# Kernel optimization log

Measured on AMD Instinct MI355X. Metric: run time of the kernel, lower is better.

The kernel has to match this reference:

```python
import jax, jax.numpy as jnp
import numpy as np

MARGIN = 0.2
EPS = 1e-8


def setup_inputs() -> dict:
    key = jax.random.key(0)
    k1, k2, k3 = jax.random.split(key, 3)
    B, D, T, C = 4096, 512, 65536, 100
    batch = jax.random.normal(k1, (B, D), dtype=jnp.float32)
    beta = jnp.ones((C,), dtype=jnp.float32) * 1.2  # learned per-class beta param
    labels = jax.random.randint(k2, (B,), 0, C)
    triplets = jax.random.randint(k3, (T, 3), 0, B)
    return {"batch": batch, "beta": beta, "labels": labels, "triplets": triplets}


def reference(batch, beta, labels, triplets):
    # Gather anchor / positive / negative embeddings: [T, D]
    a = batch[triplets[:, 0]]
    p = batch[triplets[:, 1]]
    n = batch[triplets[:, 2]]
    d_ap = jnp.sqrt(jnp.sum((a - p) ** 2, axis=-1) + EPS)  # [T]
    d_an = jnp.sqrt(jnp.sum((a - n) ** 2, axis=-1) + EPS)  # [T]
    b = beta[labels[triplets[:, 0]]]  # per-anchor-class beta, [T]
    pos_loss = jax.nn.relu(d_ap - b + MARGIN)
    neg_loss = jax.nn.relu(b - d_an + MARGIN)
    # torch bool+bool is logical OR; count triplets with any active hinge
    pair_count = jnp.sum(((pos_loss > 0.0) | (neg_loss > 0.0)).astype(jnp.float32))
    total = jnp.sum(pos_loss + neg_loss)
    loss = jnp.where(pair_count > 0.0, total / jnp.maximum(pair_count, 1.0), total)
    return loss
```

## Files before the change

kernel.cpp:

```cpp
#include <hip/hip_runtime.h>

#define MARGIN 0.2f
#define EPS_    1e-8f
#define BM 128
#define BK 64

typedef __attribute__((ext_vector_type(8))) short short8;
typedef __attribute__((ext_vector_type(4))) float f32x4;

__device__ __forceinline__ unsigned pack_bf16(float lo, float hi)
{
    union { float f; unsigned u; } a, b;
    a.f = lo; b.f = hi;
    unsigned ua = (a.u + 0x7fffu + ((a.u >> 16) & 1u)) >> 16;
    unsigned ub = (b.u + 0x7fffu + ((b.u >> 16) & 1u)) & 0xffff0000u;
    return ua | ub;
}

__global__ __launch_bounds__(256) void prep_kernel(
    const float* __restrict__ in, uint4* __restrict__ out, int n8,
    float* __restrict__ ws_total, unsigned int* __restrict__ ws_cnt)
{
    int i = blockIdx.x * blockDim.x + threadIdx.x;
    if (i == 0) { *ws_total = 0.0f; *ws_cnt = 0u; }
    if (i < n8) {
        const float4 a = ((const float4*)in)[2 * i + 0];
        const float4 b = ((const float4*)in)[2 * i + 1];
        uint4 r;
        r.x = pack_bf16(a.x, a.y);
        r.y = pack_bf16(a.z, a.w);
        r.z = pack_bf16(b.x, b.y);
        r.w = pack_bf16(b.z, b.w);
        out[i] = r;
    }
}

__global__ __launch_bounds__(256) void gemm_xxt(
    const char* __restrict__ xb,
    float* __restrict__ G, int B, int D, int NB)
{
    int lin = blockIdx.x, bm = 0, rowlen = NB;
    while (lin >= rowlen) { lin -= rowlen; ++bm; --rowlen; }
    const int bn = bm + lin;

    __shared__ char At[2][BM * BK * 2];
    __shared__ char Bt[2][BM * BK * 2];
    const int tid  = threadIdx.x;
    const int lane = tid & 63;
    const int w    = tid >> 6;
    const int wr   = w >> 1, wc = w & 1;
    const int rowb = D * 2;

    f32x4 acc[4][4] = {};

    auto stage = [&](int kk, int p) {
        #pragma unroll
        for (int c4 = 0; c4 < 4; ++c4) {
            const int c = w * 4 + c4;
            const size_t arow = (size_t)bm * BM + c * 8 + (lane >> 3);
            const size_t brow = (size_t)bn * BM + c * 8 + (lane >> 3);
            const char* asrc = xb + arow * rowb + kk * (BK * 2) + (lane & 7) * 16;
            const char* bsrc = xb + brow * rowb + kk * (BK * 2) + (lane & 7) * 16;
            __builtin_amdgcn_global_load_lds((const unsigned*)asrc,
                (unsigned*)(At[p] + c * 1024 + lane * 16), 16, 0, 0);
            __builtin_amdgcn_global_load_lds((const unsigned*)bsrc,
                (unsigned*)(Bt[p] + c * 1024 + lane * 16), 16, 0, 0);
        }
    };

    const int nk = D / BK;
    stage(0, 0);
    for (int kk = 0; kk < nk; ++kk) {
        const int p = kk & 1;
        if (kk + 1 < nk) {
            stage(kk + 1, p ^ 1);
            asm volatile("s_waitcnt vmcnt(8)" ::: "memory");
        } else {
            asm volatile("s_waitcnt vmcnt(0)" ::: "memory");
        }
        __builtin_amdgcn_s_barrier();
        __builtin_amdgcn_sched_barrier(0);

        #pragma unroll
        for (int ks = 0; ks < 2; ++ks) {
            const int kbyte = ks * 64 + (lane >> 4) * 16;
            short8 a[4], b[4];
            #pragma unroll
            for (int m = 0; m < 4; ++m) {
                const int row = wr * 64 + m * 16 + (lane & 15);
                a[m] = *(const short8*)(At[p] + row * 128 + kbyte);
            }
            #pragma unroll
            for (int n = 0; n < 4; ++n) {
                const int row = wc * 64 + n * 16 + (lane & 15);
                b[n] = *(const short8*)(Bt[p] + row * 128 + kbyte);
            }
            #pragma unroll
            for (int m = 0; m < 4; ++m)
                #pragma unroll
                for (int n = 0; n < 4; ++n)
                    acc[m][n] = __builtin_amdgcn_mfma_f32_16x16x32_bf16(
                        a[m], b[n], acc[m][n], 0, 0, 0);
        }
        asm volatile("s_waitcnt lgkmcnt(0)" ::: "memory");
        __builtin_amdgcn_sched_barrier(0);
        __builtin_amdgcn_s_barrier();
    }

    #pragma unroll
    for (int m = 0; m < 4; ++m)
        #pragma unroll
        for (int n = 0; n < 4; ++n)
            #pragma unroll
            for (int j = 0; j < 4; ++j) {
                const int row = bm * BM + wr * 64 + m * 16 + (lane >> 4) * 4 + j;
                const int col = bn * BM + wc * 64 + n * 16 + (lane & 15);
                G[(size_t)row * B + col] = acc[m][n][j];
            }
}

__global__ __launch_bounds__(256) void tri_eval(
    const float* __restrict__ G,
    const float* __restrict__ beta,
    const int*   __restrict__ labels,
    const int*   __restrict__ trip,
    int B, int T,
    float*        __restrict__ ws_total,
    unsigned int* __restrict__ ws_cnt)
{
    const int i = blockIdx.x * blockDim.x + threadIdx.x;
    float pn = 0.0f;
    int   c  = 0;
    if (i < T) {
        const int t0 = trip[3 * i + 0];
        const int t1 = trip[3 * i + 1];
        const int t2 = trip[3 * i + 2];
        const int r1 = t0 < t1 ? t0 : t1, c1 = t0 < t1 ? t1 : t0;
        const int r2 = t0 < t2 ? t0 : t2, c2 = t0 < t2 ? t2 : t0;
        const float g01 = G[(size_t)r1 * B + c1];
        const float g02 = G[(size_t)r2 * B + c2];
        const float n0  = G[(size_t)t0 * B + t0];
        const float n1  = G[(size_t)t1 * B + t1];
        const float n2  = G[(size_t)t2 * B + t2];
        const float b   = beta[labels[t0]];
        const float dap = sqrtf(fmaxf(n0 + n1 - 2.0f * g01, 0.0f) + EPS_);
        const float dan = sqrtf(fmaxf(n0 + n2 - 2.0f * g02, 0.0f) + EPS_);
        const float pos = fmaxf(dap - b + MARGIN, 0.0f);
        const float neg = fmaxf(b - dan + MARGIN, 0.0f);
        pn = pos + neg;
        c  = ((pos > 0.0f) || (neg > 0.0f)) ? 1 : 0;
    }
    #pragma unroll
    for (int off = 1; off < 64; off <<= 1) {
        pn += __shfl_xor(pn, off, 64);
        c  += __shfl_xor(c,  off, 64);
    }
    __shared__ float s_tot[4];
    __shared__ int   s_cnt[4];
    const int wid = threadIdx.x >> 6;
    if ((threadIdx.x & 63) == 0) { s_tot[wid] = pn; s_cnt[wid] = c; }
    __syncthreads();
    if (threadIdx.x == 0) {
        atomicAdd(ws_total, s_tot[0] + s_tot[1] + s_tot[2] + s_tot[3]);
        atomicAdd(ws_cnt, (unsigned)(s_cnt[0] + s_cnt[1] + s_cnt[2] + s_cnt[3]));
    }
}

__global__ __launch_bounds__(256) void triplet_loss_generic(
    const float* __restrict__ batch,
    const float* __restrict__ beta,
    const int*   __restrict__ labels,
    const int*   __restrict__ triplets,
    int T, int D,
    float*        __restrict__ ws_total,
    unsigned int* __restrict__ ws_cnt)
{
    const int lane   = threadIdx.x & 63;
    const int wid    = threadIdx.x >> 6;
    const int gwave  = (blockIdx.x * blockDim.x + threadIdx.x) >> 6;
    const int nwaves = (gridDim.x * blockDim.x) >> 6;
    const int dq     = D >> 2;

    float        tot = 0.0f;
    unsigned int cnt = 0u;

    for (int t = gwave; t < T; t += nwaves) {
        const int t0 = triplets[3 * t + 0];
        const int t1 = triplets[3 * t + 1];
        const int t2 = triplets[3 * t + 2];
        const float4* A = (const float4*)(batch + (size_t)t0 * D);
        const float4* P = (const float4*)(batch + (size_t)t1 * D);
        const float4* N = (const float4*)(batch + (size_t)t2 * D);
        float sap = 0.0f, san = 0.0f;
        for (int idx = lane; idx < dq; idx += 64) {
            const float4 av = A[idx];
            const float4 pv = P[idx];
            const float4 nv = N[idx];
            float dx = av.x - pv.x, dy = av.y - pv.y, dz = av.z - pv.z, dw = av.w - pv.w;
            sap += dx * dx + dy * dy + dz * dz + dw * dw;
            dx = av.x - nv.x; dy = av.y - nv.y; dz = av.z - nv.z; dw = av.w - nv.w;
            san += dx * dx + dy * dy + dz * dz + dw * dw;
        }
        #pragma unroll
        for (int off = 1; off < 64; off <<= 1) {
            sap += __shfl_xor(sap, off, 64);
            san += __shfl_xor(san, off, 64);
        }
        if (lane == 0) {
            const float d_ap = sqrtf(sap + EPS_);
            const float d_an = sqrtf(san + EPS_);
            const float b    = beta[labels[t0]];
            const float pos  = fmaxf(d_ap - b + MARGIN, 0.0f);
            const float neg  = fmaxf(b - d_an + MARGIN, 0.0f);
            tot += pos + neg;
            cnt += ((pos > 0.0f) || (neg > 0.0f)) ? 1u : 0u;
        }
    }

    __shared__ float        s_tot[4];
    __shared__ unsigned int s_cnt[4];
    if (lane == 0) { s_tot[wid] = tot; s_cnt[wid] = cnt; }
    __syncthreads();
    if (threadIdx.x == 0) {
        float        bt = 0.0f;
        unsigned int bc = 0u;
        const int nw = blockDim.x >> 6;
        for (int i = 0; i < nw; ++i) { bt += s_tot[i]; bc += s_cnt[i]; }
        atomicAdd(ws_total, bt);
        atomicAdd(ws_cnt, bc);
    }
}

__global__ void finalize_kernel(const float* __restrict__ ws_total,
                                const unsigned int* __restrict__ ws_cnt,
                                float* __restrict__ out)
{
    const float total = ws_total[0];
    const float pc    = (float)ws_cnt[0];
    out[0] = (pc > 0.0f) ? (total / fmaxf(pc, 1.0f)) : total;
}

extern "C" void kernel_launch(void* const* d_in, const int* in_sizes, int n_in,
                              void* d_out, int out_size, void* d_ws, size_t ws_size,
                              hipStream_t stream)
{
    const float* batch    = (const float*)d_in[0];
    const float* beta     = (const float*)d_in[1];
    const int*   labels   = (const int*)d_in[2];
    const int*   triplets = (const int*)d_in[3];

    const int B = in_sizes[2];
    const int D = in_sizes[0] / B;
    const int T = in_sizes[3] / 3;

    float*        ws_total = (float*)d_ws;
    unsigned int* ws_cnt   = (unsigned int*)((char*)d_ws + sizeof(float));

    const size_t hb_off = 32768;
    const size_t g_off  = (hb_off + (size_t)B * D * 2 + 255) & ~(size_t)255;
    const size_t need   = g_off + (size_t)B * B * 4;

    const bool fast = (B % BM == 0) && (D % BK == 0) && (ws_size >= need) && (T >= 1);

    if (fast) {
        uint4* hb = (uint4*)((char*)d_ws + hb_off);
        float* G  = (float*)((char*)d_ws + g_off);

        const int n8 = (B * D) / 8;
        prep_kernel<<<(n8 + 255) / 256, 256, 0, stream>>>(
            batch, hb, n8, ws_total, ws_cnt);

        const int NB = B / BM;
        const int nblk = NB * (NB + 1) / 2;
        gemm_xxt<<<nblk, 256, 0, stream>>>((const char*)hb, G, B, D, NB);

        tri_eval<<<(T + 255) / 256, 256, 0, stream>>>(
            G, beta, labels, triplets, B, T, ws_total, ws_cnt);
    } else {
        (void)hipMemsetAsync(d_ws, 0, 2 * sizeof(float), stream);
        const int block = 256;
        int grid = 2048;
        const int max_grid = (T + 3) / 4;
        if (grid > max_grid) grid = max_grid;
        triplet_loss_generic<<<grid, block, 0, stream>>>(
            batch, beta, labels, triplets, T, D, ws_total, ws_cnt);
    }

    finalize_kernel<<<1, 1, 0, stream>>>(ws_total, ws_cnt, (float*)d_out);
}
```

Before: 49.91 us.

## Drop GEMM double buffering and fuse finalize into triplet eval via last-block counter

The GEMM now uses a single LDS buffer and waits for each tile's loads before computing, which halves shared memory use but removes load/compute overlap. The separate finalize kernel is removed in the fast path. The last tri_eval block, detected with an atomic done counter, writes the final loss instead. This saves a kernel launch at the cost of possible exposed memory latency in the GEMM.

```diff
diff --git a/kernel.cpp b/kernel.cpp
--- a/kernel.cpp
+++ b/kernel.cpp
@@ -19,10 +19,11 @@
 
 __global__ __launch_bounds__(256) void prep_kernel(
     const float* __restrict__ in, uint4* __restrict__ out, int n8,
-    float* __restrict__ ws_total, unsigned int* __restrict__ ws_cnt)
+    float* __restrict__ ws_total, unsigned int* __restrict__ ws_cnt,
+    unsigned int* __restrict__ ws_done)
 {
     int i = blockIdx.x * blockDim.x + threadIdx.x;
-    if (i == 0) { *ws_total = 0.0f; *ws_cnt = 0u; }
+    if (i == 0) { *ws_total = 0.0f; *ws_cnt = 0u; *ws_done = 0u; }
     if (i < n8) {
         const float4 a = ((const float4*)in)[2 * i + 0];
         const float4 b = ((const float4*)in)[2 * i + 1];
@@ -43,8 +44,8 @@
     while (lin >= rowlen) { lin -= rowlen; ++bm; --rowlen; }
     const int bn = bm + lin;
 
-    __shared__ char At[2][BM * BK * 2];
-    __shared__ char Bt[2][BM * BK * 2];
+    __shared__ char At[BM * BK * 2];
+    __shared__ char Bt[BM * BK * 2];
     const int tid  = threadIdx.x;
     const int lane = tid & 63;
     const int w    = tid >> 6;
@@ -53,7 +54,8 @@
 
     f32x4 acc[4][4] = {};
 
-    auto stage = [&](int kk, int p) {
+    const int nk = D / BK;
+    for (int kk = 0; kk < nk; ++kk) {
         #pragma unroll
         for (int c4 = 0; c4 < 4; ++c4) {
             const int c = w * 4 + c4;
@@ -62,22 +64,11 @@
             const char* asrc = xb + arow * rowb + kk * (BK * 2) + (lane & 7) * 16;
             const char* bsrc = xb + brow * rowb + kk * (BK * 2) + (lane & 7) * 16;
             __builtin_amdgcn_global_load_lds((const unsigned*)asrc,
-                (unsigned*)(At[p] + c * 1024 + lane * 16), 16, 0, 0);
+                (unsigned*)(At + c * 1024 + lane * 16), 16, 0, 0);
             __builtin_amdgcn_global_load_lds((const unsigned*)bsrc,
-                (unsigned*)(Bt[p] + c * 1024 + lane * 16), 16, 0, 0);
-        }
-    };
-
-    const int nk = D / BK;
-    stage(0, 0);
-    for (int kk = 0; kk < nk; ++kk) {
-        const int p = kk & 1;
-        if (kk + 1 < nk) {
-            stage(kk + 1, p ^ 1);
-            asm volatile("s_waitcnt vmcnt(8)" ::: "memory");
-        } else {
-            asm volatile("s_waitcnt vmcnt(0)" ::: "memory");
-        }
+                (unsigned*)(Bt + c * 1024 + lane * 16), 16, 0, 0);
+        }
+        asm volatile("s_waitcnt vmcnt(0)" ::: "memory");
         __builtin_amdgcn_s_barrier();
         __builtin_amdgcn_sched_barrier(0);
 
@@ -88,12 +79,12 @@
             #pragma unroll
             for (int m = 0; m < 4; ++m) {
                 const int row = wr * 64 + m * 16 + (lane & 15);
-                a[m] = *(const short8*)(At[p] + row * 128 + kbyte);
+                a[m] = *(const short8*)(At + row * 128 + kbyte);
             }
             #pragma unroll
             for (int n = 0; n < 4; ++n) {
                 const int row = wc * 64 + n * 16 + (lane & 15);
-                b[n] = *(const short8*)(Bt[p] + row * 128 + kbyte);
+                b[n] = *(const short8*)(Bt + row * 128 + kbyte);
             }
             #pragma unroll
             for (int m = 0; m < 4; ++m)
@@ -126,7 +117,9 @@
     const int*   __restrict__ trip,
     int B, int T,
     float*        __restrict__ ws_total,
-    unsigned int* __restrict__ ws_cnt)
+    unsigned int* __restrict__ ws_cnt,
+    unsigned int* __restrict__ ws_done,
+    float*        __restrict__ out)
 {
     const int i = blockIdx.x * blockDim.x + threadIdx.x;
     float pn = 0.0f;
@@ -163,6 +156,14 @@
     if (threadIdx.x == 0) {
         atomicAdd(ws_total, s_tot[0] + s_tot[1] + s_tot[2] + s_tot[3]);
         atomicAdd(ws_cnt, (unsigned)(s_cnt[0] + s_cnt[1] + s_cnt[2] + s_cnt[3]));
+        __threadfence();
+        const unsigned done = atomicAdd(ws_done, 1u);
+        if (done == gridDim.x - 1) {
+            const float    total = atomicAdd(ws_total, 0.0f);
+            const unsigned pcnt  = atomicAdd(ws_cnt, 0u);
+            const float pc = (float)pcnt;
+            out[0] = (pc > 0.0f) ? (total / fmaxf(pc, 1.0f)) : total;
+        }
     }
 }
 
@@ -254,7 +255,8 @@
     const int T = in_sizes[3] / 3;
 
     float*        ws_total = (float*)d_ws;
-    unsigned int* ws_cnt   = (unsigned int*)((char*)d_ws + sizeof(float));
+    unsigned int* ws_cnt   = (unsigned int*)((char*)d_ws + 4);
+    unsigned int* ws_done  = (unsigned int*)((char*)d_ws + 8);
 
     const size_t hb_off = 32768;
     const size_t g_off  = (hb_off + (size_t)B * D * 2 + 255) & ~(size_t)255;
@@ -268,23 +270,23 @@
 
         const int n8 = (B * D) / 8;
         prep_kernel<<<(n8 + 255) / 256, 256, 0, stream>>>(
-            batch, hb, n8, ws_total, ws_cnt);
+            batch, hb, n8, ws_total, ws_cnt, ws_done);
 
         const int NB = B / BM;
         const int nblk = NB * (NB + 1) / 2;
         gemm_xxt<<<nblk, 256, 0, stream>>>((const char*)hb, G, B, D, NB);
 
         tri_eval<<<(T + 255) / 256, 256, 0, stream>>>(
-            G, beta, labels, triplets, B, T, ws_total, ws_cnt);
+            G, beta, labels, triplets, B, T, ws_total, ws_cnt, ws_done,
+            (float*)d_out);
     } else {
-        (void)hipMemsetAsync(d_ws, 0, 2 * sizeof(float), stream);
+        (void)hipMemsetAsync(d_ws, 0, 12, stream);
         const int block = 256;
         int grid = 2048;
         const int max_grid = (T + 3) / 4;
         if (grid > max_grid) grid = max_grid;
         triplet_loss_generic<<<grid, block, 0, stream>>>(
             batch, beta, labels, triplets, T, D, ws_total, ws_cnt);
-    }
-
-    finalize_kernel<<<1, 1, 0, stream>>>(ws_total, ws_cnt, (float*)d_out);
-}
+        finalize_kernel<<<1, 1, 0, stream>>>(ws_total, ws_cnt, (float*)d_out);
+    }
+}
```

After: 56.14 us. 12.5% more time.
